# Kernel tuning notes

Measured on AMD Instinct MI355X. Metric: run time of the kernel, lower is better.

The kernel has to match this reference:

```python
import jax, jax.numpy as jnp
import numpy as np

N = 200_000      # active voxels
C_IN = 128
C_OUT = 128
GRID = 128
K = 27           # 3x3x3 submanifold kernel offsets
EPS = 1e-4       # scn BatchNormalization default eps
LEAK = 0.333     # scn LeakyReLU default leakiness


def _build_neighbor_idx(rng):
    # unique active voxel coords via unique linear keys in GRID^3
    keys = rng.choice(GRID ** 3, size=N, replace=False).astype(np.int64)
    z = keys % GRID
    y = (keys // GRID) % GRID
    x = keys // (GRID * GRID)
    coords = np.stack([x, y, z], axis=1)  # [N,3]
    order = np.argsort(keys)
    sorted_keys = keys[order]
    offs = np.array([(dx, dy, dz) for dx in (-1, 0, 1)
                     for dy in (-1, 0, 1) for dz in (-1, 0, 1)], dtype=np.int64)
    nb = np.full((N, K), -1, dtype=np.int32)
    for k in range(K):
        q = coords + offs[k]  # [N,3]
        inb = np.all((q >= 0) & (q < GRID), axis=1)
        qk = (q[:, 0] * GRID + q[:, 1]) * GRID + q[:, 2]
        pos = np.searchsorted(sorted_keys, qk)
        pos = np.clip(pos, 0, N - 1)
        hit = inb & (sorted_keys[pos] == qk)
        nb[:, k] = np.where(hit, order[pos].astype(np.int32), -1)
    return nb


def setup_inputs() -> dict:
    key = jax.random.key(0)
    k1, k2 = jax.random.split(key)
    rng = np.random.default_rng(0)
    neighbor_idx = jnp.asarray(_build_neighbor_idx(rng))       # [N,27] int32, -1 = inactive
    features = jax.random.normal(k1, (N, C_IN), dtype=jnp.float32)
    # per-offset conv weights, scn-style init scale
    W = jax.random.normal(k2, (K, C_IN, C_OUT), dtype=jnp.float32) * (1.0 / np.sqrt(K * C_IN))
    b = jnp.zeros((C_OUT,), dtype=jnp.float32)
    gamma = jnp.ones((C_OUT,), dtype=jnp.float32)
    beta = jnp.zeros((C_OUT,), dtype=jnp.float32)
    return {"features": features, "W": W, "b": b, "gamma": gamma,
            "beta": beta, "neighbor_idx": neighbor_idx}


def reference(features, W, b, gamma, beta, neighbor_idx):
    # Submanifold 3D conv: output only at active sites; gather active neighbors.
    valid = (neighbor_idx >= 0)                      # [N,27] bool
    idx = jnp.where(valid, neighbor_idx, 0)          # safe gather index
    out = jnp.broadcast_to(b, (features.shape[0], C_OUT))
    for k in range(K):  # fixed structural loop over 27 kernel offsets
        xk = features[idx[:, k]] * valid[:, k:k + 1].astype(features.dtype)  # [N,C_IN]
        out = out + xk @ W[k]                                                # [N,C_OUT]
    # BatchNormalization over all active sites (training-mode batch stats)
    mean = jnp.mean(out, axis=0)
    var = jnp.var(out, axis=0)
    out = (out - mean) * jax.lax.rsqrt(var + EPS) * gamma + beta
    # LeakyReLU (scn default leakiness 0.333)
    return jnp.where(out > 0, out, LEAK * out)
```

## Files before the change

### kernel.cpp

```cpp
#include <hip/hip_runtime.h>
#include <hip/hip_bf16.h>

#define N_VOX 200000
#define CI 128
#define CO 128
#define KK 27
#define BM 128
#define NBLK 1563
#define NSTEP 54
#define LEAK 0.333f
#define BN_EPS 1e-4f
#define SENT 0x3FFFFu
#define ACC_STRIDE 132

typedef unsigned short u16;
typedef unsigned int u32;
typedef __attribute__((ext_vector_type(8))) short short8;
typedef __attribute__((ext_vector_type(4))) float f32x4;

typedef const __attribute__((address_space(1))) u32* gptr_t;
typedef __attribute__((address_space(3))) u32* lptr_t;

__device__ __forceinline__ u16 f2bf(float f) {
  union { float f; u32 u; } x; x.f = f;
  return (u16)((x.u + 0x7FFFu + ((x.u >> 16) & 1u)) >> 16);
}
__device__ __forceinline__ u16 cvt_bf(float f) {
  union { __hip_bfloat16 h; u16 u; } c;
  c.h = __float2bfloat16(f);
  return c.u;
}

__global__ __launch_bounds__(256) void fcast_kernel(const float* __restrict__ f,
                                                    u16* __restrict__ fb) {
  size_t i = ((size_t)blockIdx.x * 256 + threadIdx.x) * 8;
  float4 a = *(const float4*)(f + i);
  float4 b = *(const float4*)(f + i + 4);
  u16 t[8];
  t[0] = cvt_bf(a.x); t[1] = cvt_bf(a.y); t[2] = cvt_bf(a.z); t[3] = cvt_bf(a.w);
  t[4] = cvt_bf(b.x); t[5] = cvt_bf(b.y); t[6] = cvt_bf(b.z); t[7] = cvt_bf(b.w);
  *(uint4*)(fb + i) = *(const uint4*)t;
}

__global__ __launch_bounds__(256) void wcast3_kernel(const float* __restrict__ W,
                                                     u16* __restrict__ Wt3) {
  int gid = blockIdx.x * 256 + threadIdx.x;
  int lane = gid & 63, chunk = gid >> 6;
  int ks = chunk & 3, nf = (chunk >> 2) & 7, k = chunk >> 5;
  int lr = lane & 15, lg = lane >> 4;
  int co = nf * 16 + lr;
  int ci0 = ks * 32 + lg * 8;
  const float* Wk = W + (size_t)k * CI * CO;
  u16 t[8];
#pragma unroll
  for (int e = 0; e < 8; ++e) t[e] = f2bf(Wk[(ci0 + e) * CO + co]);
  *(uint4*)(Wt3 + (size_t)gid * 8) = *(const uint4*)t;
}

__global__ __launch_bounds__(256, 2) void conv_sp_kernel(
    const u16* __restrict__ featb, const u16* __restrict__ Wt3,
    const int* __restrict__ nb, const u16* __restrict__ zp,
    float* __restrict__ out, float* __restrict__ partial) {
  __shared__ __align__(16) char smem[75776];
  float* const accf = (float*)smem;
  u32* const rb_lds = (u32*)(smem + 67584);
  int* const cnt_lds = (int*)(smem + 74752);
  int* const wcnt = (int*)(smem + 74864);
  float* const ps = (float*)(smem + 67584);

  const int tid = threadIdx.x;
  const int bid = blockIdx.x;
  const int row0 = bid * BM;
  const int lane = tid & 63;
  const int w = tid >> 6;

  {
    const bool inrow = (tid < 128) && (row0 + tid < N_VOX);
    const int* nbp = nb + (size_t)(row0 + tid) * KK;
    int vv[KK];
#pragma unroll
    for (int k = 0; k < KK; ++k) vv[k] = (k != 13 && inrow) ? nbp[k] : -1;
    if (tid < 128)
      rb_lds[832 + tid] = ((u32)tid << 18) | (inrow ? (u32)(row0 + tid) : SENT);
    if (tid == 0) cnt_lds[13] = 128;
#pragma unroll
    for (int k = 0; k < KK; ++k) {
      if (k == 13) continue;
      bool valid = vv[k] >= 0;
      unsigned long long m = __ballot(valid);
      if (lane == 0) wcnt[w] = (int)__popcll(m);
      __syncthreads();
      int pos = (int)__popcll(m & ((1ull << lane) - 1ull)) + (w == 1 ? wcnt[0] : 0);
      int cnt = wcnt[0] + wcnt[1]; if (cnt > 64) cnt = 64;
      int kbase = (k < 13) ? k * 64 : 960 + (k - 14) * 64;
      if (valid && pos < 64) rb_lds[kbase + pos] = ((u32)tid << 18) | (u32)vv[k];
      int pe = (cnt + 15) & ~15;
      for (int i = cnt + tid; i < pe; i += 256) rb_lds[kbase + i] = SENT;
      if (tid == 0) cnt_lds[k] = cnt;
      __syncthreads();
    }
  }

  const int wv = w;
  const int lr = lane & 15, lg = lane >> 4;
  const int colbase = wv * 32 + lr;

  for (int kk = 0; kk < KK; ++kk) {
    const int k = (kk == 0) ? 13 : (kk <= 13 ? kk - 1 : kk);
    const int kbase = (k < 13) ? k * 64 : (k == 13 ? 832 : 960 + (k - 14) * 64);
    const int cnt = cnt_lds[k];
    if (cnt == 0) continue;
    const int nt = (cnt + 15) >> 4;
    short8 b0[4], b1[4];
    {
      const u16* wb = Wt3 + (size_t)(k * 32 + wv * 8) * 512 + lane * 8;
#pragma unroll
      for (int ks = 0; ks < 4; ++ks) {
        b0[ks] = *(const short8*)(wb + ks * 512);
        b1[ks] = *(const short8*)(wb + (4 + ks) * 512);
      }
    }
    for (int t = 0; t < nt; ++t) {
      u32 es = rb_lds[kbase + t * 16 + lr];
      u32 src = es & SENT;
      const u16* ap = (src == SENT) ? zp : (featb + (size_t)src * CI);
      short8 a[4];
#pragma unroll
      for (int ks = 0; ks < 4; ++ks) a[ks] = *(const short8*)(ap + ks * 32 + lg * 8);
      f32x4 c0 = {0.f, 0.f, 0.f, 0.f}, c1 = {0.f, 0.f, 0.f, 0.f};
#pragma unroll
      for (int ks = 0; ks < 4; ++ks) {
        c0 = __builtin_amdgcn_mfma_f32_16x16x32_bf16(a[ks], b0[ks], c0, 0, 0, 0);
        c1 = __builtin_amdgcn_mfma_f32_16x16x32_bf16(a[ks], b1[ks], c1, 0, 0, 0);
      }
      if (kk == 0) {
#pragma unroll
        for (int r = 0; r < 4; ++r) {
          int dr = (int)(rb_lds[kbase + t * 16 + lg * 4 + r] >> 18);
          accf[dr * ACC_STRIDE + colbase] = c0[r];
          accf[dr * ACC_STRIDE + colbase + 16] = c1[r];
        }
      } else {
#pragma unroll
        for (int r = 0; r < 4; ++r) {
          u32 e2 = rb_lds[kbase + t * 16 + lg * 4 + r];
          if (e2 != SENT) {
            int dr = (int)(e2 >> 18);
            accf[dr * ACC_STRIDE + colbase] += c0[r];
            accf[dr * ACC_STRIDE + colbase + 16] += c1[r];
          }
        }
      }
    }
  }
  __syncthreads();

  float s4[4] = {0.f, 0.f, 0.f, 0.f}, q4[4] = {0.f, 0.f, 0.f, 0.f};
  const int col4 = (tid & 31) * 4;
  const int rgrp = tid >> 5;
#pragma unroll
  for (int i = 0; i < 16; ++i) {
    int row = rgrp + i * 8;
    f32x4 v = *(const f32x4*)&accf[row * ACC_STRIDE + col4];
    int grow = row0 + row;
    if (grow < N_VOX) {
      *(float4*)&out[(size_t)grow * CO + col4] = *(float4*)&v;
#pragma unroll
      for (int j = 0; j < 4; ++j) { s4[j] += v[j]; q4[j] += v[j] * v[j]; }
    }
  }
  __syncthreads();
#pragma unroll
  for (int j = 0; j < 4; ++j) {
    ps[rgrp * 128 + col4 + j] = s4[j];
    ps[1024 + rgrp * 128 + col4 + j] = q4[j];
  }
  __syncthreads();
  {
    int col = tid & 127, which = tid >> 7;
    float acc = 0.f;
#pragma unroll
    for (int g = 0; g < 8; ++g) acc += ps[which * 1024 + g * 128 + col];
    partial[(size_t)bid * 256 + tid] = acc;
  }
}

__global__ __launch_bounds__(256, 2) void conv_fb_kernel(
    const float* __restrict__ feat, const u16* __restrict__ Wt3,
    const int* __restrict__ nb, float* __restrict__ out,
    float* __restrict__ partial) {
  __shared__ __align__(16) char smem[46592];
  u16* const Ab = (u16*)smem;
  int* const nbs = (int*)(smem + 32768);
  float* const sq = (float*)smem;

  const int tid = threadIdx.x;
  const int bid = blockIdx.x;
  const int row0 = bid * BM;

  for (int i = tid; i < BM * KK; i += 256) {
    int gi = row0 * KK + i;
    nbs[i] = (gi < N_VOX * KK) ? nb[gi] : -1;
  }
  __syncthreads();

  const int lane = tid & 63;
  const int wv = tid >> 6;
  const int wr = wv >> 1, wc = wv & 1;
  const int lr = lane & 15, lg = lane >> 4;
  const int arow = tid >> 1;
  const int acol = (tid & 1) * 32;

  f32x4 acc[4][4];
#pragma unroll
  for (int m = 0; m < 4; ++m)
#pragma unroll
    for (int n = 0; n < 4; ++n) acc[m][n] = (f32x4){0.f, 0.f, 0.f, 0.f};

  float4 af[8];
  short8 b0[8], b1[8];

  auto issueAf = [&](int s) {
    int k = s >> 1, half = (s & 1) * 64;
    int src = nbs[arow * KK + k];
    if (src >= 0) {
      const float4* p = (const float4*)(feat + (size_t)src * CI + half + acol);
#pragma unroll
      for (int j = 0; j < 8; ++j) af[j] = p[j];
    } else {
#pragma unroll
      for (int j = 0; j < 8; ++j) af[j] = (float4){0.f, 0.f, 0.f, 0.f};
    }
  };
  auto loadB = [&](int s, short8* bn) {
    int k = s >> 1, half = s & 1;
#pragma unroll
    for (int n = 0; n < 4; ++n)
#pragma unroll
      for (int ks = 0; ks < 2; ++ks)
        bn[n * 2 + ks] = *(const short8*)(Wt3 +
            (size_t)((k * 32 + (wc * 4 + n) * 4) + half * 2 + ks) * 512 + lane * 8);
  };
  auto writeA = [&](u16* Adst) {
    int v = arow & 7;
#pragma unroll
    for (int q = 0; q < 4; ++q) {
      u16 t8[8];
#pragma unroll
      for (int i = 0; i < 2; ++i) {
        float4 f = af[q * 2 + i];
        t8[i * 4 + 0] = cvt_bf(f.x); t8[i * 4 + 1] = cvt_bf(f.y);
        t8[i * 4 + 2] = cvt_bf(f.z); t8[i * 4 + 3] = cvt_bf(f.w);
      }
      int c_o = (tid & 1) * 4 + q;
      *(uint4*)&Adst[arow * 64 + ((c_o ^ v) << 3)] = *(const uint4*)t8;
    }
  };
  auto compute = [&](const u16* A, const short8* bc) {
#pragma unroll
    for (int ks = 0; ks < 2; ++ks) {
      short8 a[4];
#pragma unroll
      for (int m = 0; m < 4; ++m) {
        int r = wr * 64 + m * 16 + lr;
        a[m] = *(const short8*)((const char*)A + r * 128 +
                                ((ks * 64 + lg * 16) ^ ((r & 7) << 4)));
      }
#pragma unroll
      for (int m = 0; m < 4; ++m)
#pragma unroll
        for (int n = 0; n < 4; ++n)
          acc[m][n] = __builtin_amdgcn_mfma_f32_16x16x32_bf16(a[m], bc[n * 2 + ks],
                                                              acc[m][n], 0, 0, 0);
    }
  };

  issueAf(0);
  loadB(0, b0);
  for (int s = 0; s + 2 <= NSTEP - 1; s += 2) {
    writeA(Ab + (s & 1) * 8192); __syncthreads();
    issueAf(s + 1); loadB(s + 1, b1);
    compute(Ab + (s & 1) * 8192, b0);
    writeA(Ab + ((s + 1) & 1) * 8192); __syncthreads();
    issueAf(s + 2); loadB(s + 2, b0);
    compute(Ab + ((s + 1) & 1) * 8192, b1);
  }
  writeA(Ab); __syncthreads();
  issueAf(NSTEP - 1); loadB(NSTEP - 1, b1);
  compute(Ab, b0);
  writeA(Ab + 8192); __syncthreads();
  compute(Ab + 8192, b1);

  float sv[4], qv[4];
#pragma unroll
  for (int n = 0; n < 4; ++n) {
    float s = 0.f, q = 0.f;
    int col = wc * 64 + n * 16 + lr;
#pragma unroll
    for (int m = 0; m < 4; ++m) {
      int rb_ = row0 + wr * 64 + m * 16 + lg * 4;
#pragma unroll
      for (int e = 0; e < 4; ++e) {
        float x = acc[m][n][e];
        if (rb_ + e < N_VOX) out[(size_t)(rb_ + e) * CO + col] = x;
        s += x; q += x * x;
      }
    }
    s += __shfl_xor(s, 16, 64); s += __shfl_xor(s, 32, 64);
    q += __shfl_xor(q, 16, 64); q += __shfl_xor(q, 32, 64);
    sv[n] = s; qv[n] = q;
  }
  __syncthreads();
  if (lg == 0) {
#pragma unroll
    for (int n = 0; n < 4; ++n) {
      int col = wc * 64 + n * 16 + lr;
      sq[wr * 256 + col] = sv[n];
      sq[wr * 256 + 128 + col] = qv[n];
    }
  }
  __syncthreads();
  partial[(size_t)bid * 256 + tid] = sq[tid] + sq[256 + tid];
}

__global__ __launch_bounds__(256) void reduce1_kernel(const float* __restrict__ partial,
                                                      float* __restrict__ partial2) {
  int t = threadIdx.x, b = blockIdx.x;
  float acc = 0.f;
  int jend = (b + 1) * 16; if (jend > NBLK) jend = NBLK;
  for (int j = b * 16; j < jend; ++j) acc += partial[(size_t)j * 256 + t];
  partial2[(size_t)b * 256 + t] = acc;
}

__global__ __launch_bounds__(256) void reduce2_kernel(const float* __restrict__ partial2,
                                                      const float* __restrict__ gamma,
                                                      const float* __restrict__ beta,
                                                      float* __restrict__ stats) {
  __shared__ float sums[256];
  int t = threadIdx.x;
  float acc = 0.f;
  for (int j = 0; j < 98; ++j) acc += partial2[(size_t)j * 256 + t];
  sums[t] = acc;
  __syncthreads();
  if (t < 128) {
    float mean = sums[t] / (float)N_VOX;
    float var = sums[128 + t] / (float)N_VOX - mean * mean;
    float scale = gamma[t] * rsqrtf(var + BN_EPS);
    stats[t] = scale;
    stats[128 + t] = beta[t] - mean * scale;
  }
}

__global__ __launch_bounds__(256) void bnact_kernel(float* __restrict__ out,
                                                    const float* __restrict__ stats) {
  __shared__ float s_scale[128], s_shift[128];
  int t = threadIdx.x;
  if (t < 128) { s_scale[t] = stats[t]; s_shift[t] = stats[128 + t]; }
  __syncthreads();
  size_t i = (size_t)blockIdx.x * 256 + t;
  float4* o4 = (float4*)out;
  float4 v = o4[i];
  int c0 = ((int)(i & 31)) << 2;
  float x;
  x = v.x * s_scale[c0 + 0] + s_shift[c0 + 0]; v.x = x > 0.f ? x : LEAK * x;
  x = v.y * s_scale[c0 + 1] + s_shift[c0 + 1]; v.y = x > 0.f ? x : LEAK * x;
  x = v.z * s_scale[c0 + 2] + s_shift[c0 + 2]; v.z = x > 0.f ? x : LEAK * x;
  x = v.w * s_scale[c0 + 3] + s_shift[c0 + 3]; v.w = x > 0.f ? x : LEAK * x;
  o4[i] = v;
}

extern "C" void kernel_launch(void* const* d_in, const int* in_sizes, int n_in,
                              void* d_out, int out_size, void* d_ws, size_t ws_size,
                              hipStream_t stream) {
  const float* feat  = (const float*)d_in[0];
  const float* W     = (const float*)d_in[1];
  const float* gamma = (const float*)d_in[3];
  const float* beta  = (const float*)d_in[4];
  const int*   nb    = (const int*)d_in[5];
  float* out = (float*)d_out;

  char* ws = (char*)d_ws;
  u16*   Wt3      = (u16*)ws;
  float* partial  = (float*)(ws + 884736);
  float* partial2 = (float*)(ws + 2485248);
  float* stats    = (float*)(ws + 2585600);
  u16*   zp       = (u16*)(ws + 2586624);
  u16*   featb    = (u16*)(ws + 2586880);
  const size_t need_fast = 53786880u;

  hipLaunchKernelGGL(wcast3_kernel, dim3(216), dim3(256), 0, stream, W, Wt3);
  if (ws_size >= need_fast) {
    hipMemsetAsync(zp, 0, 256, stream);
    hipLaunchKernelGGL(fcast_kernel, dim3(12500), dim3(256), 0, stream, feat, featb);
    hipLaunchKernelGGL(conv_sp_kernel, dim3(NBLK), dim3(256), 0, stream,
                       featb, Wt3, nb, zp, out, partial);
  } else {
    hipLaunchKernelGGL(conv_fb_kernel, dim3(NBLK), dim3(256), 0, stream,
                       feat, Wt3, nb, out, partial);
  }
  hipLaunchKernelGGL(reduce1_kernel, dim3(98), dim3(256), 0, stream, partial, partial2);
  hipLaunchKernelGGL(reduce2_kernel, dim3(1), dim3(256), 0, stream, partial2, gamma, beta, stats);
  hipLaunchKernelGGL(bnact_kernel, dim3(25000), dim3(256), 0, stream, out, stats);
}
```

Baseline: 294.5 us.

## Flatten offset tiles into a worklist and double-buffer gathers with MFMA

Builds a per-block worklist of (offset, tile) entries in LDS so that the whole conv runs as one flat loop over 16-row tiles instead of nested offset/tile loops. The loop is software-pipelined with two register buffers, so the feature-row gathers and weight loads for the next tiles are issued before the current tile's MFMAs and LDS scatter-adds. The aim is to hide global gather latency behind compute. In exchange it zero-initialises the accumulator up front, reloads weights for every tile rather than once per offset, and raises register pressure, which may hurt occupancy at two blocks per CU.

```diff
diff --git a/kernel.cpp b/kernel.cpp
--- a/kernel.cpp
+++ b/kernel.cpp
@@ -66,6 +66,8 @@
   u32* const rb_lds = (u32*)(smem + 67584);
   int* const cnt_lds = (int*)(smem + 74752);
   int* const wcnt = (int*)(smem + 74864);
+  u32* const wl = (u32*)(smem + 74880);
+  int* const wl_n = (int*)(smem + 75360);
   float* const ps = (float*)(smem + 67584);
 
   const int tid = threadIdx.x;
@@ -73,6 +75,11 @@
   const int row0 = bid * BM;
   const int lane = tid & 63;
   const int w = tid >> 6;
+
+  {
+    f32x4 z4 = {0.f, 0.f, 0.f, 0.f};
+    for (int i = tid; i < (BM * ACC_STRIDE) / 4; i += 256) ((f32x4*)accf)[i] = z4;
+  }
 
   {
     const bool inrow = (tid < 128) && (row0 + tid < N_VOX);
@@ -101,56 +108,91 @@
     }
   }
 
+  if (tid == 0) {
+    int n = 0;
+    for (int k = 0; k < KK; ++k) {
+      int cnt = cnt_lds[k];
+      int kbase = (k < 13) ? k * 64 : (k == 13 ? 832 : 960 + (k - 14) * 64);
+      int ntk = (cnt + 15) >> 4;
+      for (int t = 0; t < ntk; ++t) wl[n++] = ((u32)k << 11) | (u32)(kbase + t * 16);
+    }
+    wl_n[0] = n;
+  }
+  __syncthreads();
+
   const int wv = w;
   const int lr = lane & 15, lg = lane >> 4;
   const int colbase = wv * 32 + lr;
-
-  for (int kk = 0; kk < KK; ++kk) {
-    const int k = (kk == 0) ? 13 : (kk <= 13 ? kk - 1 : kk);
-    const int kbase = (k < 13) ? k * 64 : (k == 13 ? 832 : 960 + (k - 14) * 64);
-    const int cnt = cnt_lds[k];
-    if (cnt == 0) continue;
-    const int nt = (cnt + 15) >> 4;
-    short8 b0[4], b1[4];
-    {
-      const u16* wb = Wt3 + (size_t)(k * 32 + wv * 8) * 512 + lane * 8;
-#pragma unroll
-      for (int ks = 0; ks < 4; ++ks) {
-        b0[ks] = *(const short8*)(wb + ks * 512);
-        b1[ks] = *(const short8*)(wb + (4 + ks) * 512);
+  const int nt = wl_n[0];
+
+  auto rbRead = [&](u32 d, u32& es, uint4& sc) {
+    int off = (int)(d & 0x7FFu);
+    es = rb_lds[off + lr];
+    sc = *(const uint4*)&rb_lds[off + lg * 4];
+  };
+  auto issueA = [&](u32 es, short8* a) {
+    u32 src = es & SENT;
+    const u16* ap = (src == SENT) ? zp : (featb + (size_t)src * CI);
+#pragma unroll
+    for (int ks = 0; ks < 4; ++ks) a[ks] = *(const short8*)(ap + ks * 32 + lg * 8);
+  };
+  auto issueB = [&](u32 d, short8* b) {
+    int k = (int)(d >> 11);
+    const u16* wb = Wt3 + (size_t)(k * 32 + wv * 8) * 512 + lane * 8;
+#pragma unroll
+    for (int j = 0; j < 8; ++j) b[j] = *(const short8*)(wb + j * 512);
+  };
+  auto computeT = [&](const short8* a, const short8* b, f32x4& c0, f32x4& c1) {
+#pragma unroll
+    for (int ks = 0; ks < 4; ++ks) {
+      c0 = __builtin_amdgcn_mfma_f32_16x16x32_bf16(a[ks], b[ks], c0, 0, 0, 0);
+      c1 = __builtin_amdgcn_mfma_f32_16x16x32_bf16(a[ks], b[4 + ks], c1, 0, 0, 0);
+    }
+  };
+  auto scat1 = [&](u32 e2, float v0, float v1) {
+    if (e2 != SENT) {
+      int dr = (int)(e2 >> 18);
+      accf[dr * ACC_STRIDE + colbase] += v0;
+      accf[dr * ACC_STRIDE + colbase + 16] += v1;
+    }
+  };
+
+  {
+    u32 es0, es1; uint4 sc0, sc1;
+    short8 a0[4], a1[4], b0v[8], b1v[8];
+    u32 d0 = wl[0], d1 = wl[1];
+    rbRead(d0, es0, sc0);
+    rbRead(d1, es1, sc1);
+    issueA(es0, a0); issueB(d0, b0v);
+    issueA(es1, a1); issueB(d1, b1v);
+    int i = 0;
+    for (; i + 1 < nt; i += 2) {
+      {
+        u32 dn = wl[(i + 2 < nt) ? i + 2 : 0];
+        u32 esn; uint4 scn; rbRead(dn, esn, scn);
+        f32x4 c0 = {0.f, 0.f, 0.f, 0.f}, c1 = {0.f, 0.f, 0.f, 0.f};
+        computeT(a0, b0v, c0, c1);
+        issueA(esn, a0); issueB(dn, b0v);
+        scat1(sc0.x, c0[0], c1[0]); scat1(sc0.y, c0[1], c1[1]);
+        scat1(sc0.z, c0[2], c1[2]); scat1(sc0.w, c0[3], c1[3]);
+        sc0 = scn;
       }
-    }
-    for (int t = 0; t < nt; ++t) {
-      u32 es = rb_lds[kbase + t * 16 + lr];
-      u32 src = es & SENT;
-      const u16* ap = (src == SENT) ? zp : (featb + (size_t)src * CI);
-      short8 a[4];
-#pragma unroll
-      for (int ks = 0; ks < 4; ++ks) a[ks] = *(const short8*)(ap + ks * 32 + lg * 8);
+      {
+        u32 dn = wl[(i + 3 < nt) ? i + 3 : 0];
+        u32 esn; uint4 scn; rbRead(dn, esn, scn);
+        f32x4 c0 = {0.f, 0.f, 0.f, 0.f}, c1 = {0.f, 0.f, 0.f, 0.f};
+        computeT(a1, b1v, c0, c1);
+        issueA(esn, a1); issueB(dn, b1v);
+        scat1(sc1.x, c0[0], c1[0]); scat1(sc1.y, c0[1], c1[1]);
+        scat1(sc1.z, c0[2], c1[2]); scat1(sc1.w, c0[3], c1[3]);
+        sc1 = scn;
+      }
+    }
+    if (i < nt) {
       f32x4 c0 = {0.f, 0.f, 0.f, 0.f}, c1 = {0.f, 0.f, 0.f, 0.f};
-#pragma unroll
-      for (int ks = 0; ks < 4; ++ks) {
-        c0 = __builtin_amdgcn_mfma_f32_16x16x32_bf16(a[ks], b0[ks], c0, 0, 0, 0);
-        c1 = __builtin_amdgcn_mfma_f32_16x16x32_bf16(a[ks], b1[ks], c1, 0, 0, 0);
-      }
-      if (kk == 0) {
-#pragma unroll
-        for (int r = 0; r < 4; ++r) {
-          int dr = (int)(rb_lds[kbase + t * 16 + lg * 4 + r] >> 18);
-          accf[dr * ACC_STRIDE + colbase] = c0[r];
-          accf[dr * ACC_STRIDE + colbase + 16] = c1[r];
-        }
-      } else {
-#pragma unroll
-        for (int r = 0; r < 4; ++r) {
-          u32 e2 = rb_lds[kbase + t * 16 + lg * 4 + r];
-          if (e2 != SENT) {
-            int dr = (int)(e2 >> 18);
-            accf[dr * ACC_STRIDE + colbase] += c0[r];
-            accf[dr * ACC_STRIDE + colbase + 16] += c1[r];
-          }
-        }
-      }
+      computeT(a0, b0v, c0, c1);
+      scat1(sc0.x, c0[0], c1[0]); scat1(sc0.y, c0[1], c1[1]);
+      scat1(sc0.z, c0[2], c1[2]); scat1(sc0.w, c0[3], c1[3]);
     }
   }
   __syncthreads();
```

Measured after the change: 256.5 us. 1.15x faster.

## Software-pipeline sparse conv with async LDS gathers over a flattened tile worklist

Applied to the files above, without the earlier changes.

The per-offset nested loop is replaced by a flattened worklist of 16-row tiles across all 27 offsets. Gathered feature rows now go asynchronously into a 4-slot LDS ring via global_load_lds with an XOR swizzle, prefetched two tiles ahead, and weight fragments are double-buffered one tile ahead. Explicit waitcnt and barriers order each stage, and the accumulator is zero-initialised up front so every tile simply accumulates. The block height drops to 96 rows with a per-offset neighbour cap of 48 and more blocks; the reduction kernels now take block counts as parameters. The aim is to hide gather latency behind MFMA work, at the cost of a per-tile block barrier and a fragile hand-set vmcnt.

```diff
diff --git a/kernel.cpp b/kernel.cpp
--- a/kernel.cpp
+++ b/kernel.cpp
@@ -5,13 +5,15 @@
 #define CI 128
 #define CO 128
 #define KK 27
-#define BM 128
-#define NBLK 1563
+#define BM 96
+#define NBLK96 2084
+#define NBLKFB 1563
 #define NSTEP 54
 #define LEAK 0.333f
 #define BN_EPS 1e-4f
 #define SENT 0x3FFFFu
 #define ACC_STRIDE 132
+#define RB_CAP 48
 
 typedef unsigned short u16;
 typedef unsigned int u32;
@@ -29,6 +31,9 @@
   union { __hip_bfloat16 h; u16 u; } c;
   c.h = __float2bfloat16(f);
   return c.u;
+}
+__device__ __forceinline__ int kbase_of(int k) {
+  return (k < 13) ? k * RB_CAP : (k == 13 ? 13 * RB_CAP : 13 * RB_CAP + 96 + (k - 14) * RB_CAP);
 }
 
 __global__ __launch_bounds__(256) void fcast_kernel(const float* __restrict__ f,
@@ -61,12 +66,15 @@
     const u16* __restrict__ featb, const u16* __restrict__ Wt3,
     const int* __restrict__ nb, const u16* __restrict__ zp,
     float* __restrict__ out, float* __restrict__ partial) {
-  __shared__ __align__(16) char smem[75776];
+  __shared__ __align__(16) char smem[73088];
   float* const accf = (float*)smem;
-  u32* const rb_lds = (u32*)(smem + 67584);
-  int* const cnt_lds = (int*)(smem + 74752);
-  int* const wcnt = (int*)(smem + 74864);
-  float* const ps = (float*)(smem + 67584);
+  u16* const ring = (u16*)(smem + 50688);
+  u32* const rb_lds = (u32*)(smem + 67072);
+  int* const cnt_lds = (int*)(smem + 72448);
+  int* const wcnt = (int*)(smem + 72560);
+  u32* const wl = (u32*)(smem + 72576);
+  int* const wl_n = (int*)(smem + 72960);
+  float* const ps = (float*)smem;
 
   const int tid = threadIdx.x;
   const int bid = blockIdx.x;
@@ -75,14 +83,19 @@
   const int w = tid >> 6;
 
   {
-    const bool inrow = (tid < 128) && (row0 + tid < N_VOX);
+    f32x4 z4 = {0.f, 0.f, 0.f, 0.f};
+    for (int i = tid; i < (BM * ACC_STRIDE) / 4; i += 256) ((f32x4*)accf)[i] = z4;
+  }
+
+  {
+    const bool inrow = (tid < BM) && (row0 + tid < N_VOX);
     const int* nbp = nb + (size_t)(row0 + tid) * KK;
     int vv[KK];
 #pragma unroll
     for (int k = 0; k < KK; ++k) vv[k] = (k != 13 && inrow) ? nbp[k] : -1;
-    if (tid < 128)
-      rb_lds[832 + tid] = ((u32)tid << 18) | (inrow ? (u32)(row0 + tid) : SENT);
-    if (tid == 0) cnt_lds[13] = 128;
+    if (tid < BM)
+      rb_lds[13 * RB_CAP + tid] = ((u32)tid << 18) | (inrow ? (u32)(row0 + tid) : SENT);
+    if (tid == 0) cnt_lds[13] = BM;
 #pragma unroll
     for (int k = 0; k < KK; ++k) {
       if (k == 13) continue;
@@ -91,66 +104,106 @@
       if (lane == 0) wcnt[w] = (int)__popcll(m);
       __syncthreads();
       int pos = (int)__popcll(m & ((1ull << lane) - 1ull)) + (w == 1 ? wcnt[0] : 0);
-      int cnt = wcnt[0] + wcnt[1]; if (cnt > 64) cnt = 64;
-      int kbase = (k < 13) ? k * 64 : 960 + (k - 14) * 64;
-      if (valid && pos < 64) rb_lds[kbase + pos] = ((u32)tid << 18) | (u32)vv[k];
+      int cnt = wcnt[0] + wcnt[1]; if (cnt > RB_CAP) cnt = RB_CAP;
+      int kb = kbase_of(k);
+      if (valid && pos < RB_CAP) rb_lds[kb + pos] = ((u32)tid << 18) | (u32)vv[k];
       int pe = (cnt + 15) & ~15;
-      for (int i = cnt + tid; i < pe; i += 256) rb_lds[kbase + i] = SENT;
+      for (int i = cnt + tid; i < pe; i += 256) rb_lds[kb + i] = SENT;
       if (tid == 0) cnt_lds[k] = cnt;
       __syncthreads();
     }
   }
+
+  if (tid == 0) {
+    int n = 0;
+    for (int k = 0; k < KK; ++k) {
+      int cnt = cnt_lds[k];
+      int kb = kbase_of(k);
+      int ntk = (cnt + 15) >> 4;
+      for (int t = 0; t < ntk; ++t) wl[n++] = ((u32)k << 11) | (u32)(kb + t * 16);
+    }
+    wl_n[0] = n;
+  }
+  __syncthreads();
 
   const int wv = w;
   const int lr = lane & 15, lg = lane >> 4;
   const int colbase = wv * 32 + lr;
-
-  for (int kk = 0; kk < KK; ++kk) {
-    const int k = (kk == 0) ? 13 : (kk <= 13 ? kk - 1 : kk);
-    const int kbase = (k < 13) ? k * 64 : (k == 13 ? 832 : 960 + (k - 14) * 64);
-    const int cnt = cnt_lds[k];
-    if (cnt == 0) continue;
-    const int nt = (cnt + 15) >> 4;
-    short8 b0[4], b1[4];
-    {
-      const u16* wb = Wt3 + (size_t)(k * 32 + wv * 8) * 512 + lane * 8;
+  const int nt = wl_n[0];
+  const int rt = w * 4 + (lane >> 4);
+  const int pc = lane & 15;
+
+  auto gldsA = [&](int j, int slot) {
+    u32 d = wl[j];
+    int off = (int)(d & 0x7FFu);
+    u32 es = rb_lds[off + rt];
+    u32 src = es & SENT;
+    const u16* g = (src == SENT) ? zp : (featb + (size_t)src * CI);
+    g += ((pc ^ rt) << 3);
+    __builtin_amdgcn_global_load_lds((gptr_t)g,
+        (lptr_t)(ring + slot * 2048 + w * 512), 16, 0, 0);
+  };
+  auto loadB = [&](int j, short8* bn) {
+    int k = (int)(wl[j] >> 11);
+    const u16* wb = Wt3 + (size_t)(k * 32 + wv * 8) * 512 + lane * 8;
+#pragma unroll
+    for (int ks = 0; ks < 4; ++ks) {
+      bn[ks] = *(const short8*)(wb + ks * 512);
+      bn[4 + ks] = *(const short8*)(wb + (4 + ks) * 512);
+    }
+  };
+  auto scat4 = [&](const uint4& sc, const f32x4& c0, const f32x4& c1) {
+    u32 e[4] = {sc.x, sc.y, sc.z, sc.w};
+#pragma unroll
+    for (int r = 0; r < 4; ++r) {
+      if (e[r] != SENT) {
+        int dr = (int)(e[r] >> 18);
+        accf[dr * ACC_STRIDE + colbase] += c0[r];
+        accf[dr * ACC_STRIDE + colbase + 16] += c1[r];
+      }
+    }
+  };
+
+  auto ITER = [&](int i, const short8* bcur, short8* bnext) {
+    gldsA((i + 2 < nt) ? i + 2 : 0, (i + 2) & 3);
+    __builtin_amdgcn_sched_barrier(0);
+    loadB((i + 1 < nt) ? i + 1 : 0, bnext);
+    __builtin_amdgcn_sched_barrier(0);
+    asm volatile("s_waitcnt vmcnt(18)" ::: "memory");
+    __builtin_amdgcn_sched_barrier(0);
+    __builtin_amdgcn_s_barrier();
+    __builtin_amdgcn_sched_barrier(0);
+    if (i < nt) {
+      u32 d = wl[i];
+      int off = (int)(d & 0x7FFu);
+      uint4 sc = *(const uint4*)&rb_lds[off + lg * 4];
+      const u16* At = ring + (i & 3) * 2048;
+      short8 a[4];
 #pragma unroll
       for (int ks = 0; ks < 4; ++ks) {
-        b0[ks] = *(const short8*)(wb + ks * 512);
-        b1[ks] = *(const short8*)(wb + (4 + ks) * 512);
-      }
-    }
-    for (int t = 0; t < nt; ++t) {
-      u32 es = rb_lds[kbase + t * 16 + lr];
-      u32 src = es & SENT;
-      const u16* ap = (src == SENT) ? zp : (featb + (size_t)src * CI);
-      short8 a[4];
-#pragma unroll
-      for (int ks = 0; ks < 4; ++ks) a[ks] = *(const short8*)(ap + ks * 32 + lg * 8);
+        int p = (ks * 4 + lg) ^ lr;
+        a[ks] = *(const short8*)(At + lr * 128 + p * 8);
+      }
       f32x4 c0 = {0.f, 0.f, 0.f, 0.f}, c1 = {0.f, 0.f, 0.f, 0.f};
 #pragma unroll
       for (int ks = 0; ks < 4; ++ks) {
-        c0 = __builtin_amdgcn_mfma_f32_16x16x32_bf16(a[ks], b0[ks], c0, 0, 0, 0);
-        c1 = __builtin_amdgcn_mfma_f32_16x16x32_bf16(a[ks], b1[ks], c1, 0, 0, 0);
-      }
-      if (kk == 0) {
-#pragma unroll
-        for (int r = 0; r < 4; ++r) {
-          int dr = (int)(rb_lds[kbase + t * 16 + lg * 4 + r] >> 18);
-          accf[dr * ACC_STRIDE + colbase] = c0[r];
-          accf[dr * ACC_STRIDE + colbase + 16] = c1[r];
-        }
-      } else {
-#pragma unroll
-        for (int r = 0; r < 4; ++r) {
-          u32 e2 = rb_lds[kbase + t * 16 + lg * 4 + r];
-          if (e2 != SENT) {
-            int dr = (int)(e2 >> 18);
-            accf[dr * ACC_STRIDE + colbase] += c0[r];
-            accf[dr * ACC_STRIDE + colbase + 16] += c1[r];
-          }
-        }
-      }
+        c0 = __builtin_amdgcn_mfma_f32_16x16x32_bf16(a[ks], bcur[ks], c0, 0, 0, 0);
+        c1 = __builtin_amdgcn_mfma_f32_16x16x32_bf16(a[ks], bcur[4 + ks], c1, 0, 0, 0);
+      }
+      scat4(sc, c0, c1);
+    }
+    __builtin_amdgcn_sched_barrier(0);
+  };
+
+  {
+    short8 b0v[8], b1v[8];
+    gldsA(0, 0);
+    gldsA(1, 1);
+    loadB(0, b0v);
+    __builtin_amdgcn_sched_barrier(0);
+    for (int i = 0; i < nt; i += 2) {
+      ITER(i, b0v, b1v);
+      ITER(i + 1, b1v, b0v);
     }
   }
   __syncthreads();
@@ -159,7 +212,7 @@
   const int col4 = (tid & 31) * 4;
   const int rgrp = tid >> 5;
 #pragma unroll
-  for (int i = 0; i < 16; ++i) {
+  for (int i = 0; i < 12; ++i) {
     int row = rgrp + i * 8;
     f32x4 v = *(const f32x4*)&accf[row * ACC_STRIDE + col4];
     int grow = row0 + row;
@@ -196,9 +249,9 @@
 
   const int tid = threadIdx.x;
   const int bid = blockIdx.x;
-  const int row0 = bid * BM;
-
-  for (int i = tid; i < BM * KK; i += 256) {
+  const int row0 = bid * 128;
+
+  for (int i = tid; i < 128 * KK; i += 256) {
     int gi = row0 * KK + i;
     nbs[i] = (gi < N_VOX * KK) ? nb[gi] : -1;
   }
@@ -324,10 +377,11 @@
 }
 
 __global__ __launch_bounds__(256) void reduce1_kernel(const float* __restrict__ partial,
-                                                      float* __restrict__ partial2) {
+                                                      float* __restrict__ partial2,
+                                                      int nblk) {
   int t = threadIdx.x, b = blockIdx.x;
   float acc = 0.f;
-  int jend = (b + 1) * 16; if (jend > NBLK) jend = NBLK;
+  int jend = (b + 1) * 16; if (jend > nblk) jend = nblk;
   for (int j = b * 16; j < jend; ++j) acc += partial[(size_t)j * 256 + t];
   partial2[(size_t)b * 256 + t] = acc;
 }
@@ -335,11 +389,11 @@
 __global__ __launch_bounds__(256) void reduce2_kernel(const float* __restrict__ partial2,
                                                       const float* __restrict__ gamma,
                                                       const float* __restrict__ beta,
-                                                      float* __restrict__ stats) {
+                                                      float* __restrict__ stats, int n2) {
   __shared__ float sums[256];
   int t = threadIdx.x;
   float acc = 0.f;
-  for (int j = 0; j < 98; ++j) acc += partial2[(size_t)j * 256 + t];
+  for (int j = 0; j < n2; ++j) acc += partial2[(size_t)j * 256 + t];
   sums[t] = acc;
   __syncthreads();
   if (t < 128) {
@@ -382,23 +436,29 @@
   char* ws = (char*)d_ws;
   u16*   Wt3      = (u16*)ws;
   float* partial  = (float*)(ws + 884736);
-  float* partial2 = (float*)(ws + 2485248);
-  float* stats    = (float*)(ws + 2585600);
-  u16*   zp       = (u16*)(ws + 2586624);
-  u16*   featb    = (u16*)(ws + 2586880);
-  const size_t need_fast = 53786880u;
+  float* partial2 = (float*)(ws + 3018752);
+  float* stats    = (float*)(ws + 3152896);
+  u16*   zp       = (u16*)(ws + 3153920);
+  u16*   featb    = (u16*)(ws + 3154176);
+  const size_t need_fast = 54354176u;
 
   hipLaunchKernelGGL(wcast3_kernel, dim3(216), dim3(256), 0, stream, W, Wt3);
   if (ws_size >= need_fast) {
     hipMemsetAsync(zp, 0, 256, stream);
     hipLaunchKernelGGL(fcast_kernel, dim3(12500), dim3(256), 0, stream, feat, featb);
-    hipLaunchKernelGGL(conv_sp_kernel, dim3(NBLK), dim3(256), 0, stream,
+    hipLaunchKernelGGL(conv_sp_kernel, dim3(NBLK96), dim3(256), 0, stream,
                        featb, Wt3, nb, zp, out, partial);
+    hipLaunchKernelGGL(reduce1_kernel, dim3(131), dim3(256), 0, stream,
+                       partial, partial2, NBLK96);
+    hipLaunchKernelGGL(reduce2_kernel, dim3(1), dim3(256), 0, stream,
+                       partial2, gamma, beta, stats, 131);
   } else {
-    hipLaunchKernelGGL(conv_fb_kernel, dim3(NBLK), dim3(256), 0, stream,
+    hipLaunchKernelGGL(conv_fb_kernel, dim3(NBLKFB), dim3(256), 0, stream,
                        feat, Wt3, nb, out, partial);
-  }
-  hipLaunchKernelGGL(reduce1_kernel, dim3(98), dim3(256), 0, stream, partial, partial2);
-  hipLaunchKernelGGL(reduce2_kernel, dim3(1), dim3(256), 0, stream, partial2, gamma, beta, stats);
+    hipLaunchKernelGGL(reduce1_kernel, dim3(98), dim3(256), 0, stream,
+                       partial, partial2, NBLKFB);
+    hipLaunchKernelGGL(reduce2_kernel, dim3(1), dim3(256), 0, stream,
+                       partial2, gamma, beta, stats, 98);
+  }
   hipLaunchKernelGGL(bnact_kernel, dim3(25000), dim3(256), 0, stream, out, stats);
 }
```

Result: no change. 298.2 us (+1.3%).
